# Performance work log

Hardware: AMD Instinct MI355X
Metric: run time of the kernel (lower is better)

## Reference

```python
import jax, jax.numpy as jnp
import numpy as np

LEVELS = ((64, 176), (32, 88), (16, 44), (8, 22))
S_TOTAL = sum(h * w for h, w in LEVELS)  # 14960
C = 128; HH = 8; HD = 16; R = 4; L = 4; P = 8
G = 32; PC_MIN = -4.0; PC_MAX = 4.0
NUM_CLASSES = 17; PROP = 3 + 3 + 4 + 1 + NUM_CLASSES  # 28


def _ln(x, g, b):
    m = x.mean(-1, keepdims=True)
    v = ((x - m) ** 2).mean(-1, keepdims=True)
    return (x - m) * jax.lax.rsqrt(v + 1e-5) * g + b


def setup_inputs() -> dict:
    key = jax.random.key(0)
    ks = jax.random.split(key, 20)
    B, N, CAM = 1, 1024, 6
    d = {}
    d['query'] = jax.random.normal(ks[0], (B, N, C), jnp.float32)
    d['gaussian_props'] = jax.random.normal(ks[1], (B, N, PROP), jnp.float32)
    d['ms_feats'] = jax.random.normal(ks[2], (B, CAM, S_TOTAL, C), jnp.float32)
    d['depth_maps'] = jax.random.uniform(ks[3], (B, CAM, 64, 176), jnp.float32, 0.5, 50.0)
    d['lidar2img'] = jax.random.normal(ks[4], (B, CAM, 4, 4), jnp.float32)
    d['img_h'] = 256
    d['img_w'] = 704
    w = lambda k, shp: jax.random.normal(k, shp, jnp.float32) * 0.02
    d['W_sc'] = w(ks[5], (3, 3, 3, C, C)); d['b_sc'] = jnp.zeros((C,), jnp.float32)
    d['sc_g'] = jnp.ones((C,), jnp.float32); d['sc_b'] = jnp.zeros((C,), jnp.float32)
    d['ref_off_w'] = w(ks[6], (C, R * 3)); d['ref_off_b'] = jnp.zeros((R * 3,), jnp.float32)
    d['off_w'] = w(ks[7], (C, HH * R * L * P * 2)); d['off_b'] = jnp.zeros((HH * R * L * P * 2,), jnp.float32)
    d['aw_w'] = w(ks[8], (C, HH * R * L * P)); d['aw_b'] = jnp.zeros((HH * R * L * P,), jnp.float32)
    d['val_w'] = w(ks[9], (C, C)); d['val_b'] = jnp.zeros((C,), jnp.float32)
    d['out_w'] = w(ks[10], (C, C)); d['out_b'] = jnp.zeros((C,), jnp.float32)
    d['an_g'] = jnp.ones((C,), jnp.float32); d['an_b'] = jnp.zeros((C,), jnp.float32)
    d['f1_w'] = w(ks[11], (C, 4 * C)); d['f1_b'] = jnp.zeros((4 * C,), jnp.float32)
    d['f2_w'] = w(ks[12], (4 * C, C)); d['f2_b'] = jnp.zeros((C,), jnp.float32)
    d['fn_g'] = jnp.ones((C,), jnp.float32); d['fn_b'] = jnp.zeros((C,), jnp.float32)
    d['p1_w'] = w(ks[13], (C, C)); d['p1_b'] = jnp.zeros((C,), jnp.float32)
    d['p2_w'] = w(ks[14], (C, PROP)); d['p2_b'] = jnp.zeros((PROP,), jnp.float32)
    return d


def _forward(query, gaussian_props, ms_feats, depth_maps, lidar2img,
             W_sc, b_sc, sc_g, sc_b, ref_off_w, ref_off_b, off_w, off_b,
             aw_w, aw_b, val_w, val_b, out_w, out_b, an_g, an_b,
             f1_w, f1_b, f2_w, f2_b, fn_g, fn_b, p1_w, p1_b, p2_w, p2_b,
             img_h, img_w):
    B, N, _ = query.shape
    CAM = ms_feats.shape[1]
    means = gaussian_props[..., :3]
    # ---- SparseConv3DBlock: scatter-mean voxelization, 3x3x3 conv, gather back ----
    vs = (PC_MAX - PC_MIN) / G
    vox = jnp.clip(jnp.floor((means - PC_MIN) / vs).astype(jnp.int32), 0, G - 1)
    flat = (vox[..., 0] * G + vox[..., 1]) * G + vox[..., 2]  # [B,N]
    bi = jnp.arange(B)[:, None]
    grid = jnp.zeros((B, G * G * G, C), query.dtype).at[bi, flat].add(query)
    cnt = jnp.zeros((B, G * G * G, 1), query.dtype).at[bi, flat].add(1.0)
    grid = (grid / jnp.maximum(cnt, 1.0)).reshape(B, G, G, G, C)
    grid = jax.lax.conv_general_dilated(grid, W_sc, (1, 1, 1), 'SAME',
                                        dimension_numbers=('NDHWC', 'DHWIO', 'NDHWC')) + b_sc
    grid = jax.nn.gelu(grid).reshape(B, G * G * G, C)
    query = _ln(query + grid[bi, flat], sc_g, sc_b)
    # ---- DeformableAttention3D ----
    fW = jnp.asarray(img_w, query.dtype); fH = jnp.asarray(img_h, query.dtype)
    ref3d = means[:, :, None, :] + (query @ ref_off_w + ref_off_b).reshape(B, N, R, 3)
    pts = jnp.concatenate([ref3d, jnp.ones_like(ref3d[..., :1])], -1)
    proj = jnp.einsum('bcij,bnrj->bcnri', lidar2img, pts)  # [B,CAM,N,R,4]
    z = proj[..., 2]; zc = jnp.maximum(z, 1e-5)
    u = proj[..., 0] / zc; v = proj[..., 1] / zc
    valid = (z > 1e-5) & (u >= 0) & (u < fW) & (v >= 0) & (v < fH)
    Hd, Wd = depth_maps.shape[2], depth_maps.shape[3]
    iu = jnp.clip((u / fW * Wd).astype(jnp.int32), 0, Wd - 1)
    iv = jnp.clip((v / fH * Hd).astype(jnp.int32), 0, Hd - 1)
    ds = jnp.take_along_axis(depth_maps.reshape(B, CAM, Hd * Wd),
                             (iv * Wd + iu).reshape(B, CAM, N * R), axis=2).reshape(B, CAM, N, R)
    wmask = jnp.exp(-jnp.abs(z - ds)) * valid.astype(query.dtype)  # [B,CAM,N,R]
    ref2 = jnp.stack([u / fW, v / fH], -1)  # [B,CAM,N,R,2]
    offs = (query @ off_w + off_b).reshape(B, N, HH, R, L, P, 2)
    attn = jax.nn.softmax((query @ aw_w + aw_b).reshape(B, N, HH, R * L * P), -1)
    attn = attn.reshape(B, N, HH, R, L, P)
    value = (ms_feats @ val_w + val_b).reshape(B, CAM, S_TOTAL, HH, HD)
    out = jnp.zeros((B, N, HH, HD), query.dtype)
    s0 = 0
    for l, (Hl, Wl) in enumerate(LEVELS):
        sz = Hl * Wl
        vl = value[:, :, s0:s0 + sz].transpose(0, 1, 3, 2, 4).reshape(B * CAM, HH, sz, HD)
        s0 += sz
        off_l = offs[:, :, :, :, l]  # [B,N,HH,R,P,2]
        loc = ref2[:, :, :, None, :, None, :] + off_l[:, None] / jnp.array([Wl, Hl], query.dtype)
        # loc: [B,CAM,N,HH,R,P,2] in normalized coords
        x = (loc[..., 0] * Wl - 0.5).transpose(0, 1, 3, 2, 4, 5).reshape(B * CAM, HH, N * R * P)
        y = (loc[..., 1] * Hl - 0.5).transpose(0, 1, 3, 2, 4, 5).reshape(B * CAM, HH, N * R * P)
        x0 = jnp.floor(x); y0 = jnp.floor(y); wx = x - x0; wy = y - y0
        x0i = jnp.clip(x0.astype(jnp.int32), 0, Wl - 1)
        x1i = jnp.clip(x0.astype(jnp.int32) + 1, 0, Wl - 1)
        y0i = jnp.clip(y0.astype(jnp.int32), 0, Hl - 1)
        y1i = jnp.clip(y0.astype(jnp.int32) + 1, 0, Hl - 1)
        g = lambda ix, iy: jnp.take_along_axis(vl, (iy * Wl + ix)[..., None], axis=2)
        samp = (((1 - wx) * (1 - wy))[..., None] * g(x0i, y0i)
                + (wx * (1 - wy))[..., None] * g(x1i, y0i)
                + ((1 - wx) * wy)[..., None] * g(x0i, y1i)
                + (wx * wy)[..., None] * g(x1i, y1i))  # [B*CAM,HH,N*R*P,HD]
        samp = samp.reshape(B, CAM, HH, N, R, P, HD)
        ws = attn[:, :, :, :, l, :][:, None].transpose(0, 1, 3, 2, 4, 5) * wmask[:, :, None, :, :, None]
        out = out + jnp.einsum('bchnrp,bchnrpd->bnhd', ws, samp)
    attn_out = out.reshape(B, N, C) @ out_w + out_b
    query = _ln(query + attn_out, an_g, an_b)
    query = _ln(query + (jax.nn.gelu(query @ f1_w + f1_b) @ f2_w + f2_b), fn_g, fn_b)
    props = gaussian_props + (jax.nn.gelu(query @ p1_w + p1_b) @ p2_w + p2_b)
    return query, props


def reference(query, gaussian_props, ms_feats, depth_maps, lidar2img,
              W_sc, b_sc, sc_g, sc_b, ref_off_w, ref_off_b, off_w, off_b,
              aw_w, aw_b, val_w, val_b, out_w, out_b, an_g, an_b,
              f1_w, f1_b, f2_w, f2_b, fn_g, fn_b, p1_w, p1_b, p2_w, p2_b,
              img_h, img_w):
    return _forward(query, gaussian_props, ms_feats, depth_maps, lidar2img,
                    W_sc, b_sc, sc_g, sc_b, ref_off_w, ref_off_b, off_w, off_b,
                    aw_w, aw_b, val_w, val_b, out_w, out_b, an_g, an_b,
                    f1_w, f1_b, f2_w, f2_b, fn_g, fn_b, p1_w, p1_b, p2_w, p2_b,
                    img_h, img_w)
```

## Files before the change

### kernel.cpp

```cpp
#include <hip/hip_runtime.h>
#include <hip/hip_bf16.h>
#include <math.h>

#define NQ    1024
#define CC    128
#define CAM   6
#define RR    4
#define LL    4
#define PP    8
#define HHD   8
#define HDD   16
#define GG    32
#define S_TOT 14960
#define PROPN 28
#define NTAP  27

typedef __attribute__((ext_vector_type(8))) short bf16x8;
typedef __attribute__((ext_vector_type(4))) float f32x4;

__device__ __forceinline__ float gelu_tanh(float x) {
    return 0.5f * x * (1.0f + tanhf(0.7978845608028654f * (x + 0.044715f * x * x * x)));
}

__device__ __forceinline__ unsigned short f2bf(float f) {
    union { float f; unsigned int u; } x; x.f = f;
    unsigned int r = (x.u + 0x7FFFu + ((x.u >> 16) & 1u)) >> 16;
    return (unsigned short)r;
}

__device__ __forceinline__ float bf2f(short s) {
    union { unsigned int u; float f; } x;
    x.u = ((unsigned int)(unsigned short)s) << 16;
    return x.f;
}

__global__ void k_wt_scatter(const float* __restrict__ Wsc, unsigned short* __restrict__ WscT,
                             const float* __restrict__ valw, unsigned short* __restrict__ valwT,
                             const float* __restrict__ outw, unsigned short* __restrict__ outwT,
                             const float* __restrict__ p1w, unsigned short* __restrict__ p1wT,
                             const float* __restrict__ f1w, unsigned short* __restrict__ f1wT,
                             const float* __restrict__ f2w, unsigned short* __restrict__ f2wT,
                             const float* __restrict__ offw, unsigned short* __restrict__ offwT,
                             const float* __restrict__ aww, unsigned short* __restrict__ awwT,
                             const float* __restrict__ p2w, unsigned short* __restrict__ p2wT,
                             const float* __restrict__ p2b, float* __restrict__ p2bp,
                             const float* __restrict__ qin, const float* __restrict__ gp,
                             float* __restrict__ grid, float* __restrict__ cnt,
                             int* __restrict__ flatidx) {
    __shared__ float t[64][65];
    __shared__ int sflat[2];
    int z = blockIdx.z;
    int tid = threadIdx.x;

    if (z >= 63) {
        int half = tid >> 7, c = tid & 127;
        int n = ((z - 63) * 4 + (blockIdx.x * 2 + blockIdx.y)) * 2 + half;
        if (c == 0) {
            float mx = gp[n * PROPN + 0], my = gp[n * PROPN + 1], mz = gp[n * PROPN + 2];
            int vx = (int)floorf((mx + 4.0f) * 4.0f);
            int vy = (int)floorf((my + 4.0f) * 4.0f);
            int vz = (int)floorf((mz + 4.0f) * 4.0f);
            vx = min(max(vx, 0), GG - 1);
            vy = min(max(vy, 0), GG - 1);
            vz = min(max(vz, 0), GG - 1);
            int f = (vx * GG + vy) * GG + vz;
            sflat[half] = f;
            flatidx[n] = f;
            atomicAdd(&cnt[f], 1.0f);
        }
        __syncthreads();
        atomicAdd(&grid[(size_t)sflat[half] * CC + c], qin[(size_t)n * CC + c]);
        return;
    }

    int n0 = blockIdx.x * 64, k0 = blockIdx.y * 64;
    if (z == 62) {
#pragma unroll
        for (int it = 0; it < 16; ++it) {
            int idx = tid + it * 256;
            int r = idx >> 6, c = idx & 63;
            t[r][c] = (n0 + c < PROPN) ? p2w[(size_t)(k0 + r) * PROPN + n0 + c] : 0.f;
        }
        __syncthreads();
#pragma unroll
        for (int it = 0; it < 16; ++it) {
            int idx = tid + it * 256;
            int r = idx >> 6, c = idx & 63;
            p2wT[(size_t)(n0 + r) * 128 + k0 + c] = f2bf(t[c][r]);
        }
        if (blockIdx.x == 0 && blockIdx.y == 0 && tid < 128)
            p2bp[tid] = (tid < PROPN) ? p2b[tid] : 0.f;
        return;
    }
    const float* src; unsigned short* dst; int ss, ds;
    if (z < 27)       { src = Wsc + (size_t)z * 16384; dst = WscT + (size_t)z * 16384; ss = 128; ds = 128; }
    else if (z == 27) { src = valw; dst = valwT; ss = 128; ds = 128; }
    else if (z == 28) { src = outw; dst = outwT; ss = 128; ds = 128; }
    else if (z == 29) { src = p1w;  dst = p1wT;  ss = 128; ds = 128; }
    else if (z < 34)  { int q = z - 30; src = f1w + q * 128; dst = f1wT + (size_t)q * 16384; ss = 512;  ds = 128; }
    else if (z < 38)  { int q = z - 34; src = f2w + (size_t)q * 16384; dst = f2wT + q * 128; ss = 128;  ds = 512; }
    else if (z < 54)  { int q = z - 38; src = offw + q * 128; dst = offwT + (size_t)q * 16384; ss = 2048; ds = 128; }
    else              { int q = z - 54; src = aww + q * 128;  dst = awwT + (size_t)q * 16384; ss = 1024; ds = 128; }
#pragma unroll
    for (int it = 0; it < 16; ++it) {
        int idx = tid + it * 256;
        int r = idx >> 6, c = idx & 63;
        t[r][c] = src[(size_t)(k0 + r) * ss + n0 + c];
    }
    __syncthreads();
#pragma unroll
    for (int it = 0; it < 16; ++it) {
        int idx = tid + it * 256;
        int r = idx >> 6, c = idx & 63;
        dst[(size_t)(n0 + r) * ds + k0 + c] = f2bf(t[c][r]);
    }
}

__global__ __launch_bounds__(256) void k_conv1m(
    const float* __restrict__ grid, const float* __restrict__ cnt,
    const int* __restrict__ flatidx, const unsigned short* __restrict__ WT,
    float* __restrict__ convacc27) {
    __shared__ bf16x8 As[128 * 16];
    __shared__ bf16x8 Bs[128 * 16];
    __shared__ int   nbase[128];
    __shared__ float nscale[128];
    int tid = threadIdx.x;
    int tap = blockIdx.y;
    int q0 = blockIdx.x * 128;
    int dz = tap / 9 - 1, dy = (tap / 3) % 3 - 1, dx = tap % 3 - 1;

    if (tid < 128) {
        int f = flatidx[q0 + tid];
        int nx = (f >> 10) + dz, ny = ((f >> 5) & 31) + dy, nz = (f & 31) + dx;
        bool ok = (nx >= 0 && nx < GG && ny >= 0 && ny < GG && nz >= 0 && nz < GG);
        int nf = ok ? (nx * GG + ny) * GG + nz : 0;
        nbase[tid] = nf;
        nscale[tid] = ok ? 1.0f / fmaxf(cnt[nf], 1.0f) : 0.f;
    }
    __syncthreads();
#pragma unroll
    for (int it = 0; it < 8; ++it) {
        int idx = tid + it * 256;
        int m = idx >> 4, c = idx & 15;
        const float* p = grid + (size_t)nbase[m] * CC + c * 8;
        float s = nscale[m];
        float4 a = *(const float4*)p;
        float4 b = *(const float4*)(p + 4);
        bf16x8 u;
        u[0] = (short)f2bf(a.x * s); u[1] = (short)f2bf(a.y * s);
        u[2] = (short)f2bf(a.z * s); u[3] = (short)f2bf(a.w * s);
        u[4] = (short)f2bf(b.x * s); u[5] = (short)f2bf(b.y * s);
        u[6] = (short)f2bf(b.z * s); u[7] = (short)f2bf(b.w * s);
        As[m * 16 + (c ^ (m & 15))] = u;
    }
    const unsigned short* Wt = WT + (size_t)tap * CC * CC;
#pragma unroll
    for (int it = 0; it < 8; ++it) {
        int idx = tid + it * 256;
        int n = idx >> 4, c = idx & 15;
        bf16x8 w = *(const bf16x8*)(Wt + (size_t)n * CC + c * 8);
        Bs[n * 16 + (c ^ (n & 15))] = w;
    }
    __syncthreads();

    int lane = tid & 63, wv = tid >> 6;
    int wr = (wv >> 1) * 64, wc = (wv & 1) * 64;
    int r = lane & 15, q = lane >> 4;
    f32x4 acc[4][4];
#pragma unroll
    for (int i = 0; i < 4; ++i)
#pragma unroll
        for (int j = 0; j < 4; ++j)
#pragma unroll
            for (int e = 0; e < 4; ++e) acc[i][j][e] = 0.f;
#pragma unroll
    for (int ks = 0; ks < 4; ++ks) {
        bf16x8 bfr[4];
#pragma unroll
        for (int j = 0; j < 4; ++j)
            bfr[j] = Bs[(wc + j * 16 + r) * 16 + ((ks * 4 + q) ^ r)];
#pragma unroll
        for (int i = 0; i < 4; ++i) {
            bf16x8 af = As[(wr + i * 16 + r) * 16 + ((ks * 4 + q) ^ r)];
#pragma unroll
            for (int j = 0; j < 4; ++j)
                acc[i][j] = __builtin_amdgcn_mfma_f32_16x16x32_bf16(af, bfr[j], acc[i][j], 0, 0, 0);
        }
    }
    float* dst = convacc27 + (size_t)tap * NQ * CC;
#pragma unroll
    for (int i = 0; i < 4; ++i)
#pragma unroll
        for (int e = 0; e < 4; ++e) {
            int m = q0 + wr + i * 16 + q * 4 + e;
#pragma unroll
            for (int j = 0; j < 4; ++j) {
                int col = wc + j * 16 + r;
                dst[(size_t)m * CC + col] = acc[i][j][e];
            }
        }
}

__global__ void k_ln_conv_proj(const float* __restrict__ a, const float* __restrict__ convacc27,
                               const float* __restrict__ bconv,
                               const float* __restrict__ g, const float* __restrict__ be,
                               float* __restrict__ out,
                               const float* __restrict__ refw, const float* __restrict__ refb,
                               const float* __restrict__ gp, const float* __restrict__ l2i,
                               const float* __restrict__ depth,
                               const int* __restrict__ ih, const int* __restrict__ iw,
                               float* __restrict__ wm, float* __restrict__ r2u,
                               float* __restrict__ r2v) {
    int n = blockIdx.x, c = threadIdx.x;
    float apart = 0.f;
#pragma unroll
    for (int t = 0; t < NTAP; ++t) apart += convacc27[((size_t)t * NQ + n) * CC + c];
    float x = a[n * CC + c] + gelu_tanh(apart + bconv[c]);
    __shared__ float w4[4];
    __shared__ float qrow[CC];
    __shared__ float ro[12];
    float s = x;
#pragma unroll
    for (int d = 1; d < 64; d <<= 1) s += __shfl_xor(s, d);
    if ((c & 63) == 0) w4[c >> 6] = s;
    __syncthreads();
    float m = (w4[0] + w4[1]) * (1.0f / CC);
    float dd = x - m;
    float v = dd * dd;
#pragma unroll
    for (int d = 1; d < 64; d <<= 1) v += __shfl_xor(v, d);
    if ((c & 63) == 0) w4[2 + (c >> 6)] = v;
    __syncthreads();
    float var = (w4[2] + w4[3]) * (1.0f / CC);
    float qv = dd * rsqrtf(var + 1e-5f) * g[c] + be[c];
    out[n * CC + c] = qv;
    qrow[c] = qv;
    __syncthreads();
    if (c < 12) {
        float sacc = refb[c];
#pragma unroll 4
        for (int k = 0; k < 128; ++k) sacc += qrow[k] * refw[k * 12 + c];
        ro[c] = sacc;
    }
    __syncthreads();
    if (c < 24) {
        int cam = c >> 2, r = c & 3;
        float fH = (float)(*ih), fW = (float)(*iw);
        const float* M = l2i + cam * 16;
        float px = gp[n * PROPN + 0] + ro[r * 3 + 0];
        float py = gp[n * PROPN + 1] + ro[r * 3 + 1];
        float pz = gp[n * PROPN + 2] + ro[r * 3 + 2];
        float p0 = M[0] * px + M[1] * py + M[2]  * pz + M[3];
        float p1 = M[4] * px + M[5] * py + M[6]  * pz + M[7];
        float p2 = M[8] * px + M[9] * py + M[10] * pz + M[11];
        float zc = fmaxf(p2, 1e-5f);
        float u = p0 / zc, vv = p1 / zc;
        bool valid = (p2 > 1e-5f) && (u >= 0.f) && (u < fW) && (vv >= 0.f) && (vv < fH);
        int iu = min(max((int)(u / fW * 176.f), 0), 175);
        int iv = min(max((int)(vv / fH * 64.f), 0), 63);
        float ds = depth[cam * 64 * 176 + iv * 176 + iu];
        int o = cam * (NQ * RR) + n * RR + r;
        wm[o]  = valid ? expf(-fabsf(p2 - ds)) : 0.f;
        r2u[o] = u / fW;
        r2v[o] = vv / fH;
    }
}

__global__ __launch_bounds__(256) void k_qhead(
    const float* __restrict__ A,
    const unsigned short* __restrict__ offwT, const float* __restrict__ offb,
    unsigned short* __restrict__ offsb,
    const unsigned short* __restrict__ awwT, const float* __restrict__ awb,
    unsigned short* __restrict__ attn)
{
    __shared__ bf16x8 Bs[128 * 16];
    bool isoff = blockIdx.x < 16;
    int n0 = (isoff ? blockIdx.x : (blockIdx.x - 16)) * 128;
    const unsigned short* WT = isoff ? offwT : awwT;
    int m0 = blockIdx.y * 128;
    int tid = threadIdx.x, lane = tid & 63, wv = tid >> 6;
    int r = lane & 15, q = lane >> 4;
    int mw = m0 + wv * 32;

#pragma unroll
    for (int it = 0; it < 8; ++it) {
        int idx = tid + it * 256;
        int n = idx >> 4, c = idx & 15;
        Bs[n * 16 + (c ^ (n & 15))] = *(const bf16x8*)(WT + (size_t)(n0 + n) * 128 + c * 8);
    }
    __syncthreads();

    f32x4 acc[2][8];
#pragma unroll
    for (int i = 0; i < 2; ++i)
#pragma unroll
        for (int j = 0; j < 8; ++j)
#pragma unroll
            for (int e = 0; e < 4; ++e) acc[i][j][e] = 0.f;

#pragma unroll
    for (int ks = 0; ks < 4; ++ks) {
        bf16x8 af[2];
#pragma unroll
        for (int i = 0; i < 2; ++i) {
            const float* p = A + (size_t)(mw + i * 16 + r) * 128 + (ks * 4 + q) * 8;
            float4 a = *(const float4*)p;
            float4 b = *(const float4*)(p + 4);
            bf16x8 u;
            u[0] = (short)f2bf(a.x); u[1] = (short)f2bf(a.y);
            u[2] = (short)f2bf(a.z); u[3] = (short)f2bf(a.w);
            u[4] = (short)f2bf(b.x); u[5] = (short)f2bf(b.y);
            u[6] = (short)f2bf(b.z); u[7] = (short)f2bf(b.w);
            af[i] = u;
        }
#pragma unroll
        for (int j = 0; j < 8; ++j) {
            bf16x8 b = Bs[(j * 16 + r) * 16 + ((ks * 4 + q) ^ r)];
#pragma unroll
            for (int i = 0; i < 2; ++i)
                acc[i][j] = __builtin_amdgcn_mfma_f32_16x16x32_bf16(af[i], b, acc[i][j], 0, 0, 0);
        }
    }

    float bia[8];
    const float* bsrc = isoff ? offb : awb;
#pragma unroll
    for (int j = 0; j < 8; ++j) bia[j] = bsrc[n0 + j * 16 + r];

    if (isoff) {
#pragma unroll
        for (int i = 0; i < 2; ++i)
#pragma unroll
            for (int e = 0; e < 4; ++e) {
                int m = mw + i * 16 + q * 4 + e;
                unsigned short* orow = offsb + (size_t)m * 2048 + n0;
#pragma unroll
                for (int j = 0; j < 8; ++j)
                    orow[j * 16 + r] = f2bf(acc[i][j][e] + bia[j]);
            }
    } else {
#pragma unroll
        for (int i = 0; i < 2; ++i)
#pragma unroll
            for (int e = 0; e < 4; ++e) {
                float mx = -1e30f;
#pragma unroll
                for (int j = 0; j < 8; ++j) mx = fmaxf(mx, acc[i][j][e] + bia[j]);
#pragma unroll
                for (int d = 1; d < 16; d <<= 1) mx = fmaxf(mx, __shfl_xor(mx, d));
                float ex[8];
                float sum = 0.f;
#pragma unroll
                for (int j = 0; j < 8; ++j) { ex[j] = expf(acc[i][j][e] + bia[j] - mx); sum += ex[j]; }
#pragma unroll
                for (int d = 1; d < 16; d <<= 1) sum += __shfl_xor(sum, d);
                float inv = 1.0f / sum;
                int m = mw + i * 16 + q * 4 + e;
                unsigned short* orow = attn + (size_t)m * 1024 + n0;
#pragma unroll
                for (int j = 0; j < 8; ++j)
                    orow[j * 16 + r] = f2bf(ex[j] * inv);
            }
    }
}

__global__ __launch_bounds__(256) void k_valproj(
    const float* __restrict__ A, const unsigned short* __restrict__ WT,
    const float* __restrict__ bias, unsigned short* __restrict__ out, int M)
{
    __shared__ bf16x8 Bs[128 * 16];
    __shared__ unsigned short Os[64 * 128];
    __shared__ float sbias[128];
    int tid = threadIdx.x;
    int m0 = blockIdx.x * 64;
    int lane = tid & 63, wv = tid >> 6;
    int r = lane & 15, q = lane >> 4;

#pragma unroll
    for (int it = 0; it < 8; ++it) {
        int idx = tid + it * 256;
        int n = idx >> 4, c = idx & 15;
        Bs[n * 16 + (c ^ (n & 15))] = *(const bf16x8*)(WT + (size_t)n * 128 + c * 8);
    }
    if (tid < 128) sbias[tid] = bias[tid];
    __syncthreads();

    int row = m0 + wv * 16 + r;
    int mg = min(row, M - 1);
    const float* pA = A + (size_t)mg * 128;

    f32x4 acc[8];
#pragma unroll
    for (int j = 0; j < 8; ++j)
#pragma unroll
        for (int e = 0; e < 4; ++e) acc[j][e] = 0.f;

#pragma unroll
    for (int ks = 0; ks < 4; ++ks) {
        const float* p = pA + ks * 32 + q * 8;
        float4 a = *(const float4*)p;
        float4 b = *(const float4*)(p + 4);
        bf16x8 af;
        af[0] = (short)f2bf(a.x); af[1] = (short)f2bf(a.y);
        af[2] = (short)f2bf(a.z); af[3] = (short)f2bf(a.w);
        af[4] = (short)f2bf(b.x); af[5] = (short)f2bf(b.y);
        af[6] = (short)f2bf(b.z); af[7] = (short)f2bf(b.w);
        bf16x8 bfr[8];
#pragma unroll
        for (int j = 0; j < 8; ++j)
            bfr[j] = Bs[(j * 16 + r) * 16 + ((ks * 4 + q) ^ r)];
#pragma unroll
        for (int j = 0; j < 8; ++j)
            acc[j] = __builtin_amdgcn_mfma_f32_16x16x32_bf16(af, bfr[j], acc[j], 0, 0, 0);
    }

#pragma unroll
    for (int j = 0; j < 8; ++j)
#pragma unroll
        for (int e = 0; e < 4; ++e) {
            int rl = wv * 16 + q * 4 + e;
            Os[rl * 128 + j * 16 + r] = f2bf(acc[j][e] + sbias[j * 16 + r]);
        }
    __syncthreads();
#pragma unroll
    for (int it = 0; it < 4; ++it) {
        int idx = tid + it * 256;
        int rl = idx >> 4, ch = idx & 15;
        int m = m0 + rl;
        if (m < M)
            *(bf16x8*)(out + (size_t)m * 128 + ch * 8) = *(const bf16x8*)&Os[rl * 128 + ch * 8];
    }
}

__global__ void k_sample(const unsigned short* __restrict__ value,
                         const unsigned short* __restrict__ offsb,
                         const unsigned short* __restrict__ attn,
                         const float* __restrict__ wm,
                         const float* __restrict__ r2u, const float* __restrict__ r2v,
                         float* __restrict__ sampout) {
    const int Wl_[4] = {176, 88, 44, 22};
    const int Hl_[4] = {64, 32, 16, 8};
    const int s0_[4] = {0, 11264, 14080, 14784};
    int n = blockIdx.x, tid = threadIdx.x;
    __shared__ float s_attn[1024];
    __shared__ float s_offs[2048];
    __shared__ float s_wm[24], s_ru[24], s_rv[24];

    if (tid < 128) {
        bf16x8 v = *(const bf16x8*)(attn + (size_t)n * 1024 + tid * 8);
#pragma unroll
        for (int d = 0; d < 8; ++d) s_attn[tid * 8 + d] = bf2f(v[d]);
    }
    {
        bf16x8 v = *(const bf16x8*)(offsb + (size_t)n * 2048 + tid * 8);
#pragma unroll
        for (int d = 0; d < 8; ++d) s_offs[tid * 8 + d] = bf2f(v[d]);
    }
    if (tid < 24) {
        int cam = tid >> 2, r = tid & 3;
        int o = cam * (NQ * RR) + n * RR + r;
        s_wm[tid] = wm[o]; s_ru[tid] = r2u[o]; s_rv[tid] = r2v[o];
    }
    __syncthreads();

    int h = tid >> 5, slot = tid & 31;
    int l = slot >> 3, p = slot & 7;
    int Wl = Wl_[l], Hl = Hl_[l];
    float fWl = (float)Wl, fHl = (float)Hl;
    float acc[16];
#pragma unroll
    for (int d = 0; d < 16; ++d) acc[d] = 0.f;

    for (int cr = 0; cr < 24; ++cr) {
        int cam = cr >> 2, r = cr & 3;
        float ws = s_attn[h * 128 + r * 32 + l * 8 + p] * s_wm[cr];
        if (ws == 0.f) continue;
        float ox = s_offs[h * 256 + r * 64 + l * 16 + p * 2 + 0];
        float oy = s_offs[h * 256 + r * 64 + l * 16 + p * 2 + 1];
        float x = s_ru[cr] * fWl + ox - 0.5f;
        float y = s_rv[cr] * fHl + oy - 0.5f;
        float xf = floorf(x), yf = floorf(y);
        float wx = x - xf, wy = y - yf;
        int x0 = min(max((int)xf, 0), Wl - 1);
        int x1 = min(max((int)xf + 1, 0), Wl - 1);
        int y0 = min(max((int)yf, 0), Hl - 1);
        int y1 = min(max((int)yf + 1, 0), Hl - 1);
        size_t b = ((size_t)cam * S_TOT + s0_[l]) * CC + h * HDD;
        const unsigned short* p00 = value + b + (size_t)(y0 * Wl + x0) * CC;
        const unsigned short* p01 = value + b + (size_t)(y0 * Wl + x1) * CC;
        const unsigned short* p10 = value + b + (size_t)(y1 * Wl + x0) * CC;
        const unsigned short* p11 = value + b + (size_t)(y1 * Wl + x1) * CC;
        float w00 = ws * (1.f - wx) * (1.f - wy);
        float w01 = ws * wx * (1.f - wy);
        float w10 = ws * (1.f - wx) * wy;
        float w11 = ws * wx * wy;
        bf16x8 va0 = *(const bf16x8*)p00, va1 = *(const bf16x8*)(p00 + 8);
        bf16x8 vb0 = *(const bf16x8*)p01, vb1 = *(const bf16x8*)(p01 + 8);
        bf16x8 vc0 = *(const bf16x8*)p10, vc1 = *(const bf16x8*)(p10 + 8);
        bf16x8 vd0 = *(const bf16x8*)p11, vd1 = *(const bf16x8*)(p11 + 8);
#pragma unroll
        for (int d = 0; d < 8; ++d)
            acc[d] += w00 * bf2f(va0[d]) + w01 * bf2f(vb0[d]) + w10 * bf2f(vc0[d]) + w11 * bf2f(vd0[d]);
#pragma unroll
        for (int d = 0; d < 8; ++d)
            acc[8 + d] += w00 * bf2f(va1[d]) + w01 * bf2f(vb1[d]) + w10 * bf2f(vc1[d]) + w11 * bf2f(vd1[d]);
    }

#pragma unroll
    for (int d = 0; d < 16; ++d) {
        float a = acc[d];
#pragma unroll
        for (int s = 16; s >= 1; s >>= 1) a += __shfl_xor(a, s, 32);
        acc[d] = a;
    }
    if (slot == 0) {
#pragma unroll
        for (int d = 0; d < 16; ++d)
            sampout[(size_t)n * CC + h * HDD + d] = acc[d];
    }
}

__global__ __launch_bounds__(256) void k_tail(
    const float* __restrict__ sampout,
    const unsigned short* __restrict__ outwT, const float* __restrict__ outb,
    const float* __restrict__ q1, const float* __restrict__ ang, const float* __restrict__ anb,
    const unsigned short* __restrict__ f1wT, const float* __restrict__ f1b,
    const unsigned short* __restrict__ f2wT, const float* __restrict__ f2b,
    const float* __restrict__ fng, const float* __restrict__ fnb,
    const unsigned short* __restrict__ p1wT, const float* __restrict__ p1b,
    const unsigned short* __restrict__ p2wT, const float* __restrict__ p2bp,
    const float* __restrict__ gp, float* __restrict__ outq, float* __restrict__ outp)
{
    __shared__ bf16x8 As[16 * 16];
    __shared__ bf16x8 Aff[16 * 64];
    __shared__ float xrow[16 * 128];
    __shared__ float q2s[16 * 128];
    unsigned short* Affu = (unsigned short*)Aff;
    unsigned short* As2u = (unsigned short*)Aff;
    int tid = threadIdx.x, m0 = blockIdx.x * 16;
    int lane = tid & 63, wv = tid >> 6;
    int wc = wv * 32;
    int r = lane & 15, q = lane >> 4;
    int lrow = tid >> 4, ls = tid & 15;

    bf16x8 b1[2][4];
#pragma unroll
    for (int j = 0; j < 2; ++j)
#pragma unroll
        for (int ks = 0; ks < 4; ++ks)
            b1[j][ks] = *(const bf16x8*)(outwT + (size_t)(wc + j * 16 + r) * 128 + (ks * 4 + q) * 8);

    {
        int m = tid >> 4, c = tid & 15;
        const float* p = sampout + (size_t)(m0 + m) * 128 + c * 8;
        float4 a = *(const float4*)p;
        float4 b = *(const float4*)(p + 4);
        bf16x8 u;
        u[0] = (short)f2bf(a.x); u[1] = (short)f2bf(a.y);
        u[2] = (short)f2bf(a.z); u[3] = (short)f2bf(a.w);
        u[4] = (short)f2bf(b.x); u[5] = (short)f2bf(b.y);
        u[6] = (short)f2bf(b.z); u[7] = (short)f2bf(b.w);
        As[m * 16 + (c ^ m)] = u;
    }
    __syncthreads();

    f32x4 acc[2];
    bf16x8 a4[4];
#pragma unroll
    for (int ks = 0; ks < 4; ++ks) a4[ks] = As[r * 16 + ((ks * 4 + q) ^ r)];
#pragma unroll
    for (int j = 0; j < 2; ++j)
#pragma unroll
        for (int e = 0; e < 4; ++e) acc[j][e] = 0.f;
#pragma unroll
    for (int ks = 0; ks < 4; ++ks)
#pragma unroll
        for (int j = 0; j < 2; ++j)
            acc[j] = __builtin_amdgcn_mfma_f32_16x16x32_bf16(a4[ks], b1[j][ks], acc[j], 0, 0, 0);
#pragma unroll
    for (int e = 0; e < 4; ++e) {
        int ml = q * 4 + e;
#pragma unroll
        for (int j = 0; j < 2; ++j) {
            int cl = wc + j * 16 + r;
            xrow[ml * 128 + cl] = acc[j][e] + outb[cl] + q1[(size_t)(m0 + ml) * 128 + cl];
        }
    }
    __syncthreads();

    {
        float* xr = xrow + lrow * 128;
        float sum = 0.f;
#pragma unroll
        for (int e = ls; e < 128; e += 16) sum += xr[e];
#pragma unroll
        for (int d = 8; d; d >>= 1) sum += __shfl_xor(sum, d, 16);
        float mean = sum * (1.0f / 128.0f);
        float var = 0.f;
#pragma unroll
        for (int e = ls; e < 128; e += 16) { float dd = xr[e] - mean; var += dd * dd; }
#pragma unroll
        for (int d = 8; d; d >>= 1) var += __shfl_xor(var, d, 16);
        float rstd = rsqrtf(var * (1.0f / 128.0f) + 1e-5f);
#pragma unroll
        for (int e = ls; e < 128; e += 16)
            q2s[lrow * 128 + e] = (xr[e] - mean) * rstd * ang[e] + anb[e];
    }
    __syncthreads();
    {
        int m = tid >> 4, c = tid & 15;
        const float* p = q2s + m * 128 + c * 8;
        bf16x8 u;
#pragma unroll
        for (int d = 0; d < 8; ++d) u[d] = (short)f2bf(p[d]);
        As[m * 16 + (c ^ m)] = u;
    }
    __syncthreads();

#pragma unroll
    for (int ks = 0; ks < 4; ++ks) a4[ks] = As[r * 16 + ((ks * 4 + q) ^ r)];
    bf16x8 bcur[2][4];
#pragma unroll
    for (int j = 0; j < 2; ++j)
#pragma unroll
        for (int ks = 0; ks < 4; ++ks)
            bcur[j][ks] = *(const bf16x8*)(f1wT + (size_t)(wc + j * 16 + r) * 128 + (ks * 4 + q) * 8);
#pragma unroll
    for (int nt = 0; nt < 4; ++nt) {
        bf16x8 bnx[2][4];
        if (nt < 3) {
#pragma unroll
            for (int j = 0; j < 2; ++j)
#pragma unroll
                for (int ks = 0; ks < 4; ++ks)
                    bnx[j][ks] = *(const bf16x8*)(f1wT + (size_t)(nt + 1) * 16384
                                                  + (size_t)(wc + j * 16 + r) * 128 + (ks * 4 + q) * 8);
        }
#pragma unroll
        for (int j = 0; j < 2; ++j)
#pragma unroll
            for (int e = 0; e < 4; ++e) acc[j][e] = 0.f;
#pragma unroll
        for (int ks = 0; ks < 4; ++ks)
#pragma unroll
            for (int j = 0; j < 2; ++j)
                acc[j] = __builtin_amdgcn_mfma_f32_16x16x32_bf16(a4[ks], bcur[j][ks], acc[j], 0, 0, 0);
#pragma unroll
        for (int e = 0; e < 4; ++e) {
            int ml = q * 4 + e;
#pragma unroll
            for (int j = 0; j < 2; ++j) {
                int col = nt * 128 + wc + j * 16 + r;
                float v = gelu_tanh(acc[j][e] + f1b[col]);
                Affu[(ml * 64 + ((col >> 3) ^ ml)) * 8 + (col & 7)] = f2bf(v);
            }
        }
        if (nt < 3) {
#pragma unroll
            for (int j = 0; j < 2; ++j)
#pragma unroll
                for (int ks = 0; ks < 4; ++ks) bcur[j][ks] = bnx[j][ks];
        }
    }
    __syncthreads();

#pragma unroll
    for (int j = 0; j < 2; ++j)
#pragma unroll
        for (int e = 0; e < 4; ++e) acc[j][e] = 0.f;
#pragma unroll
    for (int j = 0; j < 2; ++j)
#pragma unroll
        for (int ks = 0; ks < 4; ++ks)
            bcur[j][ks] = *(const bf16x8*)(f2wT + (size_t)(wc + j * 16 + r) * 512 + (ks * 4 + q) * 8);
#pragma unroll
    for (int kc = 0; kc < 4; ++kc) {
        bf16x8 bnx[2][4];
        if (kc < 3) {
#pragma unroll
            for (int j = 0; j < 2; ++j)
#pragma unroll
                for (int ks = 0; ks < 4; ++ks)
                    bnx[j][ks] = *(const bf16x8*)(f2wT + (size_t)(wc + j * 16 + r) * 512
                                                  + ((kc + 1) * 16 + ks * 4 + q) * 8);
        }
#pragma unroll
        for (int ks = 0; ks < 4; ++ks) {
            bf16x8 af = Aff[r * 64 + ((kc * 16 + ks * 4 + q) ^ r)];
#pragma unroll
            for (int j = 0; j < 2; ++j)
                acc[j] = __builtin_amdgcn_mfma_f32_16x16x32_bf16(af, bcur[j][ks], acc[j], 0, 0, 0);
        }
        if (kc < 3) {
#pragma unroll
            for (int j = 0; j < 2; ++j)
#pragma unroll
                for (int ks = 0; ks < 4; ++ks) bcur[j][ks] = bnx[j][ks];
        }
    }
#pragma unroll
    for (int e = 0; e < 4; ++e) {
        int ml = q * 4 + e;
#pragma unroll
        for (int j = 0; j < 2; ++j) {
            int cl = wc + j * 16 + r;
            xrow[ml * 128 + cl] = acc[j][e] + f2b[cl] + q2s[ml * 128 + cl];
        }
    }
    __syncthreads();

    {
        float* xr = xrow + lrow * 128;
        float sum = 0.f;
#pragma unroll
        for (int e = ls; e < 128; e += 16) sum += xr[e];
#pragma unroll
        for (int d = 8; d; d >>= 1) sum += __shfl_xor(sum, d, 16);
        float mean = sum * (1.0f / 128.0f);
        float var = 0.f;
#pragma unroll
        for (int e = ls; e < 128; e += 16) { float dd = xr[e] - mean; var += dd * dd; }
#pragma unroll
        for (int d = 8; d; d >>= 1) var += __shfl_xor(var, d, 16);
        float rstd = rsqrtf(var * (1.0f / 128.0f) + 1e-5f);
        float* oq = outq + (size_t)(m0 + lrow) * 128;
#pragma unroll
        for (int e = ls; e < 128; e += 16) {
            float v = (xr[e] - mean) * rstd * fng[e] + fnb[e];
            oq[e] = v;
            q2s[lrow * 128 + e] = v;
        }
    }
    __syncthreads();
    {
        int m = tid >> 4, c = tid & 15;
        const float* p = q2s + m * 128 + c * 8;
        bf16x8 u;
#pragma unroll
        for (int d = 0; d < 8; ++d) u[d] = (short)f2bf(p[d]);
        As[m * 16 + (c ^ m)] = u;
    }
    __syncthreads();

#pragma unroll
    for (int ks = 0; ks < 4; ++ks) a4[ks] = As[r * 16 + ((ks * 4 + q) ^ r)];
#pragma unroll
    for (int j = 0; j < 2; ++j) {
#pragma unroll
        for (int ks = 0; ks < 4; ++ks)
            bcur[j][ks] = *(const bf16x8*)(p1wT + (size_t)(wc + j * 16 + r) * 128 + (ks * 4 + q) * 8);
#pragma unroll
        for (int e = 0; e < 4; ++e) acc[j][e] = 0.f;
    }
#pragma unroll
    for (int j = 0; j < 2; ++j)
#pragma unroll
        for (int ks = 0; ks < 4; ++ks)
            b1[j][ks] = *(const bf16x8*)(p2wT + (size_t)(wc + j * 16 + r) * 128 + (ks * 4 + q) * 8);
#pragma unroll
    for (int ks = 0; ks < 4; ++ks)
#pragma unroll
        for (int j = 0; j < 2; ++j)
            acc[j] = __builtin_amdgcn_mfma_f32_16x16x32_bf16(a4[ks], bcur[j][ks], acc[j], 0, 0, 0);
#pragma unroll
    for (int e = 0; e < 4; ++e) {
        int ml = q * 4 + e;
#pragma unroll
        for (int j = 0; j < 2; ++j) {
            int cl = wc + j * 16 + r;
            float v = gelu_tanh(acc[j][e] + p1b[cl]);
            As2u[(ml * 16 + ((cl >> 3) ^ ml)) * 8 + (cl & 7)] = f2bf(v);
        }
    }
    __syncthreads();

#pragma unroll
    for (int j = 0; j < 2; ++j)
#pragma unroll
        for (int e = 0; e < 4; ++e) acc[j][e] = 0.f;
#pragma unroll
    for (int ks = 0; ks < 4; ++ks) {
        bf16x8 af = Aff[r * 16 + ((ks * 4 + q) ^ r)];
#pragma unroll
        for (int j = 0; j < 2; ++j)
            acc[j] = __builtin_amdgcn_mfma_f32_16x16x32_bf16(af, b1[j][ks], acc[j], 0, 0, 0);
    }
#pragma unroll
    for (int e = 0; e < 4; ++e) {
        int m = m0 + q * 4 + e;
#pragma unroll
        for (int j = 0; j < 2; ++j) {
            int cl = wc + j * 16 + r;
            if (cl < PROPN)
                outp[(size_t)m * PROPN + cl] = acc[j][e] + p2bp[cl] + gp[(size_t)m * PROPN + cl];
        }
    }
}

extern "C" void kernel_launch(void* const* d_in, const int* in_sizes, int n_in,
                              void* d_out, int out_size, void* d_ws, size_t ws_size,
                              hipStream_t stream) {
    const float* query = (const float*)d_in[0];
    const float* gp    = (const float*)d_in[1];
    const float* ms    = (const float*)d_in[2];
    const float* depth = (const float*)d_in[3];
    const float* l2i   = (const float*)d_in[4];
    const int*   ih    = (const int*)d_in[5];
    const int*   iw    = (const int*)d_in[6];
    const float* Wsc   = (const float*)d_in[7];
    const float* bsc   = (const float*)d_in[8];
    const float* scg   = (const float*)d_in[9];
    const float* scb   = (const float*)d_in[10];
    const float* refw  = (const float*)d_in[11];
    const float* refb  = (const float*)d_in[12];
    const float* offw  = (const float*)d_in[13];
    const float* offbi = (const float*)d_in[14];
    const float* aww   = (const float*)d_in[15];
    const float* awb   = (const float*)d_in[16];
    const float* valw  = (const float*)d_in[17];
    const float* valb  = (const float*)d_in[18];
    const float* outw  = (const float*)d_in[19];
    const float* outb  = (const float*)d_in[20];
    const float* ang   = (const float*)d_in[21];
    const float* anb   = (const float*)d_in[22];
    const float* f1w   = (const float*)d_in[23];
    const float* f1b   = (const float*)d_in[24];
    const float* f2w   = (const float*)d_in[25];
    const float* f2b   = (const float*)d_in[26];
    const float* fng   = (const float*)d_in[27];
    const float* fnb   = (const float*)d_in[28];
    const float* p1w   = (const float*)d_in[29];
    const float* p1b   = (const float*)d_in[30];
    const float* p2w   = (const float*)d_in[31];
    const float* p2b   = (const float*)d_in[32];

    float* outq = (float*)d_out;
    float* outp = outq + NQ * CC;

    float* ws = (float*)d_ws;
    size_t o = 0;
    float* grid    = ws + o; o += (size_t)GG * GG * GG * CC;
    float* cnt     = ws + o; o += GG * GG * GG;
    size_t zero_floats = o;
    int*   flatidx = (int*)(ws + o); o += NQ;
    float* convacc27 = ws + o; o += (size_t)NTAP * NQ * CC;
    float* q1      = ws + o; o += NQ * CC;
    float* wm      = ws + o; o += CAM * NQ * RR;
    float* r2u     = ws + o; o += CAM * NQ * RR;
    float* r2v     = ws + o; o += CAM * NQ * RR;
    float* sampout = ws + o; o += NQ * CC;
    float* p2bp    = ws + o; o += 128;
    unsigned short* u16base = (unsigned short*)(ws + o);
    size_t uo = 0;
    unsigned short* value = u16base + uo; uo += (size_t)CAM * S_TOT * CC;
    unsigned short* offsb = u16base + uo; uo += (size_t)NQ * 2048;
    unsigned short* attn  = u16base + uo; uo += (size_t)NQ * 1024;
    unsigned short* offwT = u16base + uo; uo += (size_t)2048 * 128;
    unsigned short* awwT  = u16base + uo; uo += (size_t)1024 * 128;
    unsigned short* valwT = u16base + uo; uo += 128 * 128;
    unsigned short* outwT = u16base + uo; uo += 128 * 128;
    unsigned short* f1wT  = u16base + uo; uo += 512 * 128;
    unsigned short* f2wT  = u16base + uo; uo += 128 * 512;
    unsigned short* p1wT  = u16base + uo; uo += 128 * 128;
    unsigned short* p2wT  = u16base + uo; uo += 128 * 128;
    unsigned short* WscT  = u16base + uo; uo += (size_t)27 * 128 * 128;
    (void)ws_size; (void)in_sizes; (void)n_in; (void)out_size;

    hipMemsetAsync(ws, 0, zero_floats * sizeof(float), stream);

    k_wt_scatter<<<dim3(2, 2, 63 + 128), 256, 0, stream>>>(
        Wsc, WscT, valw, valwT, outw, outwT, p1w, p1wT, f1w, f1wT, f2w, f2wT,
        offw, offwT, aww, awwT, p2w, p2wT, p2b, p2bp,
        query, gp, grid, cnt, flatidx);

    k_conv1m<<<dim3(8, 27), 256, 0, stream>>>(grid, cnt, flatidx, WscT, convacc27);
    k_ln_conv_proj<<<NQ, CC, 0, stream>>>(query, convacc27, bsc, scg, scb, q1,
                                          refw, refb, gp, l2i, depth, ih, iw, wm, r2u, r2v);

    k_qhead<<<dim3(24, 8), 256, 0, stream>>>(q1, offwT, offbi, offsb, awwT, awb, attn);
    k_valproj<<<(CAM * S_TOT + 63) / 64, 256, 0, stream>>>(ms, valwT, valb, value, CAM * S_TOT);
    k_sample<<<NQ, 256, 0, stream>>>(value, offsb, attn, wm, r2u, r2v, sampout);

    k_tail<<<64, 256, 0, stream>>>(sampout, outwT, outb, q1, ang, anb,
                                   f1wT, f1b, f2wT, f2b, fng, fnb,
                                   p1wT, p1b, p2wT, p2bp, gp, outq, outp);
}
```

Before: 227.5 us.

## Fuse value projection into weight-prep kernel and split sampling across camera halves

```diff
diff --git a/kernel.cpp b/kernel.cpp
--- a/kernel.cpp
+++ b/kernel.cpp
@@ -14,6 +14,9 @@
 #define S_TOT 14960
 #define PROPN 28
 #define NTAP  27
+#define MVAL  (CAM * S_TOT)
+#define NVB   ((MVAL + 63) / 64)
+#define ZWT   191
 
 typedef __attribute__((ext_vector_type(8))) short bf16x8;
 typedef __attribute__((ext_vector_type(4))) float f32x4;
@@ -34,8 +37,9 @@
     return x.f;
 }
 
-__global__ void k_wt_scatter(const float* __restrict__ Wsc, unsigned short* __restrict__ WscT,
-                             const float* __restrict__ valw, unsigned short* __restrict__ valwT,
+__global__ __launch_bounds__(256) void k_wt_scatter(
+                             const float* __restrict__ Wsc, unsigned short* __restrict__ WscT,
+                             const float* __restrict__ valw,
                              const float* __restrict__ outw, unsigned short* __restrict__ outwT,
                              const float* __restrict__ p1w, unsigned short* __restrict__ p1wT,
                              const float* __restrict__ f1w, unsigned short* __restrict__ f1wT,
@@ -46,11 +50,82 @@
                              const float* __restrict__ p2b, float* __restrict__ p2bp,
                              const float* __restrict__ qin, const float* __restrict__ gp,
                              float* __restrict__ grid, float* __restrict__ cnt,
-                             int* __restrict__ flatidx) {
-    __shared__ float t[64][65];
+                             int* __restrict__ flatidx,
+                             const float* __restrict__ ms, const float* __restrict__ valb,
+                             unsigned short* __restrict__ value) {
+    __shared__ union SM {
+        float t[64][65];
+        struct { bf16x8 Bs[128 * 16]; unsigned short Os[64 * 128]; float sbias[128]; } v;
+    } sm;
     __shared__ int sflat[2];
     int z = blockIdx.z;
     int tid = threadIdx.x;
+
+    if (z >= ZWT) {
+        int vb = (z - ZWT) * 4 + blockIdx.x * 2 + blockIdx.y;
+        if (vb >= NVB) return;
+        int m0 = vb * 64;
+        int lane = tid & 63, wv = tid >> 6;
+        int r = lane & 15, q = lane >> 4;
+        unsigned int* Bsw = (unsigned int*)sm.v.Bs;
+#pragma unroll
+        for (int it = 0; it < 32; ++it) {
+            int idx = tid + it * 256;
+            int k = (idx >> 7) * 2, nn = idx & 127;
+            unsigned int lo = f2bf(valw[k * 128 + nn]);
+            unsigned int hi = f2bf(valw[(k + 1) * 128 + nn]);
+            Bsw[(nn * 16 + ((k >> 3) ^ (nn & 15))) * 4 + ((k >> 1) & 3)] = lo | (hi << 16);
+        }
+        if (tid < 128) sm.v.sbias[tid] = valb[tid];
+        __syncthreads();
+
+        int row = m0 + wv * 16 + r;
+        int mg = min(row, MVAL - 1);
+        const float* pA = ms + (size_t)mg * 128;
+
+        f32x4 acc[8];
+#pragma unroll
+        for (int j = 0; j < 8; ++j)
+#pragma unroll
+            for (int e = 0; e < 4; ++e) acc[j][e] = 0.f;
+
+#pragma unroll
+        for (int ks = 0; ks < 4; ++ks) {
+            const float* p = pA + ks * 32 + q * 8;
+            float4 a = *(const float4*)p;
+            float4 b = *(const float4*)(p + 4);
+            bf16x8 af;
+            af[0] = (short)f2bf(a.x); af[1] = (short)f2bf(a.y);
+            af[2] = (short)f2bf(a.z); af[3] = (short)f2bf(a.w);
+            af[4] = (short)f2bf(b.x); af[5] = (short)f2bf(b.y);
+            af[6] = (short)f2bf(b.z); af[7] = (short)f2bf(b.w);
+            bf16x8 bfr[8];
+#pragma unroll
+            for (int j = 0; j < 8; ++j)
+                bfr[j] = sm.v.Bs[(j * 16 + r) * 16 + ((ks * 4 + q) ^ r)];
+#pragma unroll
+            for (int j = 0; j < 8; ++j)
+                acc[j] = __builtin_amdgcn_mfma_f32_16x16x32_bf16(af, bfr[j], acc[j], 0, 0, 0);
+        }
+
+#pragma unroll
+        for (int j = 0; j < 8; ++j)
+#pragma unroll
+            for (int e = 0; e < 4; ++e) {
+                int rl = wv * 16 + q * 4 + e;
+                sm.v.Os[rl * 128 + j * 16 + r] = f2bf(acc[j][e] + sm.v.sbias[j * 16 + r]);
+            }
+        __syncthreads();
+#pragma unroll
+        for (int it = 0; it < 4; ++it) {
+            int idx = tid + it * 256;
+            int rl = idx >> 4, ch = idx & 15;
+            int m = m0 + rl;
+            if (m < MVAL)
+                *(bf16x8*)(value + (size_t)m * 128 + ch * 8) = *(const bf16x8*)&sm.v.Os[rl * 128 + ch * 8];
+        }
+        return;
+    }
 
     if (z >= 63) {
         int half = tid >> 7, c = tid & 127;
@@ -79,14 +154,14 @@
         for (int it = 0; it < 16; ++it) {
             int idx = tid + it * 256;
             int r = idx >> 6, c = idx & 63;
-            t[r][c] = (n0 + c < PROPN) ? p2w[(size_t)(k0 + r) * PROPN + n0 + c] : 0.f;
+            sm.t[r][c] = (n0 + c < PROPN) ? p2w[(size_t)(k0 + r) * PROPN + n0 + c] : 0.f;
         }
         __syncthreads();
 #pragma unroll
         for (int it = 0; it < 16; ++it) {
             int idx = tid + it * 256;
             int r = idx >> 6, c = idx & 63;
-            p2wT[(size_t)(n0 + r) * 128 + k0 + c] = f2bf(t[c][r]);
+            p2wT[(size_t)(n0 + r) * 128 + k0 + c] = f2bf(sm.t[c][r]);
         }
         if (blockIdx.x == 0 && blockIdx.y == 0 && tid < 128)
             p2bp[tid] = (tid < PROPN) ? p2b[tid] : 0.f;
@@ -94,25 +169,25 @@
     }
     const float* src; unsigned short* dst; int ss, ds;
     if (z < 27)       { src = Wsc + (size_t)z * 16384; dst = WscT + (size_t)z * 16384; ss = 128; ds = 128; }
-    else if (z == 27) { src = valw; dst = valwT; ss = 128; ds = 128; }
-    else if (z == 28) { src = outw; dst = outwT; ss = 128; ds = 128; }
-    else if (z == 29) { src = p1w;  dst = p1wT;  ss = 128; ds = 128; }
-    else if (z < 34)  { int q = z - 30; src = f1w + q * 128; dst = f1wT + (size_t)q * 16384; ss = 512;  ds = 128; }
-    else if (z < 38)  { int q = z - 34; src = f2w + (size_t)q * 16384; dst = f2wT + q * 128; ss = 128;  ds = 512; }
-    else if (z < 54)  { int q = z - 38; src = offw + q * 128; dst = offwT + (size_t)q * 16384; ss = 2048; ds = 128; }
-    else              { int q = z - 54; src = aww + q * 128;  dst = awwT + (size_t)q * 16384; ss = 1024; ds = 128; }
+    else if (z == 27) { src = outw; dst = outwT; ss = 128; ds = 128; }
+    else if (z == 28) { src = p1w;  dst = p1wT;  ss = 128; ds = 128; }
+    else if (z == 29) { int q = z - 29; src = f1w + q * 128; dst = f1wT + (size_t)q * 16384; ss = 512; ds = 128; }
+    else if (z < 33)  { int q = z - 29; src = f1w + q * 128; dst = f1wT + (size_t)q * 16384; ss = 512;  ds = 128; }
+    else if (z < 37)  { int q = z - 33; src = f2w + (size_t)q * 16384; dst = f2wT + q * 128; ss = 128;  ds = 512; }
+    else if (z < 53)  { int q = z - 37; src = offw + q * 128; dst = offwT + (size_t)q * 16384; ss = 2048; ds = 128; }
+    else              { int q = z - 53; src = aww + q * 128;  dst = awwT + (size_t)q * 16384; ss = 1024; ds = 128; }
 #pragma unroll
     for (int it = 0; it < 16; ++it) {
         int idx = tid + it * 256;
         int r = idx >> 6, c = idx & 63;
-        t[r][c] = src[(size_t)(k0 + r) * ss + n0 + c];
+        sm.t[r][c] = src[(size_t)(k0 + r) * ss + n0 + c];
     }
     __syncthreads();
 #pragma unroll
     for (int it = 0; it < 16; ++it) {
         int idx = tid + it * 256;
         int r = idx >> 6, c = idx & 63;
-        dst[(size_t)(n0 + r) * ds + k0 + c] = f2bf(t[c][r]);
+        dst[(size_t)(n0 + r) * ds + k0 + c] = f2bf(sm.t[c][r]);
     }
 }
 
@@ -204,7 +279,7 @@
 __global__ void k_ln_conv_proj(const float* __restrict__ a, const float* __restrict__ convacc27,
                                const float* __restrict__ bconv,
                                const float* __restrict__ g, const float* __restrict__ be,
-                               float* __restrict__ out,
+                               float* __restrict__ out, unsigned short* __restrict__ outbf,
                                const float* __restrict__ refw, const float* __restrict__ refb,
                                const float* __restrict__ gp, const float* __restrict__ l2i,
                                const float* __restrict__ depth,
@@ -234,6 +309,7 @@
     float var = (w4[2] + w4[3]) * (1.0f / CC);
     float qv = dd * rsqrtf(var + 1e-5f) * g[c] + be[c];
     out[n * CC + c] = qv;
+    outbf[n * CC + c] = f2bf(qv);
     qrow[c] = qv;
     __syncthreads();
     if (c < 12) {
@@ -267,7 +343,7 @@
 }
 
 __global__ __launch_bounds__(256) void k_qhead(
-    const float* __restrict__ A,
+    const unsigned short* __restrict__ Abf,
     const unsigned short* __restrict__ offwT, const float* __restrict__ offb,
     unsigned short* __restrict__ offsb,
     const unsigned short* __restrict__ awwT, const float* __restrict__ awb,
@@ -302,17 +378,8 @@
     for (int ks = 0; ks < 4; ++ks) {
         bf16x8 af[2];
 #pragma unroll
-        for (int i = 0; i < 2; ++i) {
-            const float* p = A + (size_t)(mw + i * 16 + r) * 128 + (ks * 4 + q) * 8;
-            float4 a = *(const float4*)p;
-            float4 b = *(const float4*)(p + 4);
-            bf16x8 u;
-            u[0] = (short)f2bf(a.x); u[1] = (short)f2bf(a.y);
-            u[2] = (short)f2bf(a.z); u[3] = (short)f2bf(a.w);
-            u[4] = (short)f2bf(b.x); u[5] = (short)f2bf(b.y);
-            u[6] = (short)f2bf(b.z); u[7] = (short)f2bf(b.w);
-            af[i] = u;
-        }
+        for (int i = 0; i < 2; ++i)
+            af[i] = *(const bf16x8*)(Abf + (size_t)(mw + i * 16 + r) * 128 + (ks * 4 + q) * 8);
 #pragma unroll
         for (int j = 0; j < 8; ++j) {
             bf16x8 b = Bs[(j * 16 + r) * 16 + ((ks * 4 + q) ^ r)];
@@ -364,75 +431,8 @@
     }
 }
 
-__global__ __launch_bounds__(256) void k_valproj(
-    const float* __restrict__ A, const unsigned short* __restrict__ WT,
-    const float* __restrict__ bias, unsigned short* __restrict__ out, int M)
-{
-    __shared__ bf16x8 Bs[128 * 16];
-    __shared__ unsigned short Os[64 * 128];
-    __shared__ float sbias[128];
-    int tid = threadIdx.x;
-    int m0 = blockIdx.x * 64;
-    int lane = tid & 63, wv = tid >> 6;
-    int r = lane & 15, q = lane >> 4;
-
-#pragma unroll
-    for (int it = 0; it < 8; ++it) {
-        int idx = tid + it * 256;
-        int n = idx >> 4, c = idx & 15;
-        Bs[n * 16 + (c ^ (n & 15))] = *(const bf16x8*)(WT + (size_t)n * 128 + c * 8);
-    }
-    if (tid < 128) sbias[tid] = bias[tid];
-    __syncthreads();
-
-    int row = m0 + wv * 16 + r;
-    int mg = min(row, M - 1);
-    const float* pA = A + (size_t)mg * 128;
-
-    f32x4 acc[8];
-#pragma unroll
-    for (int j = 0; j < 8; ++j)
-#pragma unroll
-        for (int e = 0; e < 4; ++e) acc[j][e] = 0.f;
-
-#pragma unroll
-    for (int ks = 0; ks < 4; ++ks) {
-        const float* p = pA + ks * 32 + q * 8;
-        float4 a = *(const float4*)p;
-        float4 b = *(const float4*)(p + 4);
-        bf16x8 af;
-        af[0] = (short)f2bf(a.x); af[1] = (short)f2bf(a.y);
-        af[2] = (short)f2bf(a.z); af[3] = (short)f2bf(a.w);
-        af[4] = (short)f2bf(b.x); af[5] = (short)f2bf(b.y);
-        af[6] = (short)f2bf(b.z); af[7] = (short)f2bf(b.w);
-        bf16x8 bfr[8];
-#pragma unroll
-        for (int j = 0; j < 8; ++j)
-            bfr[j] = Bs[(j * 16 + r) * 16 + ((ks * 4 + q) ^ r)];
-#pragma unroll
-        for (int j = 0; j < 8; ++j)
-            acc[j] = __builtin_amdgcn_mfma_f32_16x16x32_bf16(af, bfr[j], acc[j], 0, 0, 0);
-    }
-
-#pragma unroll
-    for (int j = 0; j < 8; ++j)
-#pragma unroll
-        for (int e = 0; e < 4; ++e) {
-            int rl = wv * 16 + q * 4 + e;
-            Os[rl * 128 + j * 16 + r] = f2bf(acc[j][e] + sbias[j * 16 + r]);
-        }
-    __syncthreads();
-#pragma unroll
-    for (int it = 0; it < 4; ++it) {
-        int idx = tid + it * 256;
-        int rl = idx >> 4, ch = idx & 15;
-        int m = m0 + rl;
-        if (m < M)
-            *(bf16x8*)(out + (size_t)m * 128 + ch * 8) = *(const bf16x8*)&Os[rl * 128 + ch * 8];
-    }
-}
-
-__global__ void k_sample(const unsigned short* __restrict__ value,
+__global__ __launch_bounds__(512) void k_sample(
+                         const unsigned short* __restrict__ value,
                          const unsigned short* __restrict__ offsb,
                          const unsigned short* __restrict__ attn,
                          const float* __restrict__ wm,
@@ -445,13 +445,14 @@
     __shared__ float s_attn[1024];
     __shared__ float s_offs[2048];
     __shared__ float s_wm[24], s_ru[24], s_rv[24];
+    __shared__ float part[HHD][HDD];
 
     if (tid < 128) {
         bf16x8 v = *(const bf16x8*)(attn + (size_t)n * 1024 + tid * 8);
 #pragma unroll
         for (int d = 0; d < 8; ++d) s_attn[tid * 8 + d] = bf2f(v[d]);
     }
-    {
+    if (tid < 256) {
         bf16x8 v = *(const bf16x8*)(offsb + (size_t)n * 2048 + tid * 8);
 #pragma unroll
         for (int d = 0; d < 8; ++d) s_offs[tid * 8 + d] = bf2f(v[d]);
@@ -463,7 +464,9 @@
     }
     __syncthreads();
 
-    int h = tid >> 5, slot = tid & 31;
+    int half = tid >> 8;
+    int t8 = tid & 255;
+    int h = t8 >> 5, slot = t8 & 31;
     int l = slot >> 3, p = slot & 7;
     int Wl = Wl_[l], Hl = Hl_[l];
     float fWl = (float)Wl, fHl = (float)Hl;
@@ -471,7 +474,7 @@
 #pragma unroll
     for (int d = 0; d < 16; ++d) acc[d] = 0.f;
 
-    for (int cr = 0; cr < 24; ++cr) {
+    for (int cr = half * 12; cr < half * 12 + 12; ++cr) {
         int cam = cr >> 2, r = cr & 3;
         float ws = s_attn[h * 128 + r * 32 + l * 8 + p] * s_wm[cr];
         if (ws == 0.f) continue;
@@ -513,10 +516,15 @@
         for (int s = 16; s >= 1; s >>= 1) a += __shfl_xor(a, s, 32);
         acc[d] = a;
     }
-    if (slot == 0) {
+    if (half == 1 && slot == 0) {
+#pragma unroll
+        for (int d = 0; d < 16; ++d) part[h][d] = acc[d];
+    }
+    __syncthreads();
+    if (half == 0 && slot == 0) {
 #pragma unroll
         for (int d = 0; d < 16; ++d)
-            sampout[(size_t)n * CC + h * HDD + d] = acc[d];
+            sampout[(size_t)n * CC + h * HDD + d] = acc[d] + part[h][d];
     }
 }
 
@@ -855,9 +863,9 @@
     unsigned short* value = u16base + uo; uo += (size_t)CAM * S_TOT * CC;
     unsigned short* offsb = u16base + uo; uo += (size_t)NQ * 2048;
     unsigned short* attn  = u16base + uo; uo += (size_t)NQ * 1024;
+    unsigned short* q1bf  = u16base + uo; uo += (size_t)NQ * CC;
     unsigned short* offwT = u16base + uo; uo += (size_t)2048 * 128;
     unsigned short* awwT  = u16base + uo; uo += (size_t)1024 * 128;
-    unsigned short* valwT = u16base + uo; uo += 128 * 128;
     unsigned short* outwT = u16base + uo; uo += 128 * 128;
     unsigned short* f1wT  = u16base + uo; uo += 512 * 128;
     unsigned short* f2wT  = u16base + uo; uo += 128 * 512;
@@ -868,18 +876,19 @@
 
     hipMemsetAsync(ws, 0, zero_floats * sizeof(float), stream);
 
-    k_wt_scatter<<<dim3(2, 2, 63 + 128), 256, 0, stream>>>(
-        Wsc, WscT, valw, valwT, outw, outwT, p1w, p1wT, f1w, f1wT, f2w, f2wT,
+    int zvp = (NVB + 3) / 4;
+    k_wt_scatter<<<dim3(2, 2, ZWT + zvp), 256, 0, stream>>>(
+        Wsc, WscT, valw, outw, outwT, p1w, p1wT, f1w, f1wT, f2w, f2wT,
         offw, offwT, aww, awwT, p2w, p2wT, p2b, p2bp,
-        query, gp, grid, cnt, flatidx);
+        query, gp, grid, cnt, flatidx,
+        ms, valb, value);
 
     k_conv1m<<<dim3(8, 27), 256, 0, stream>>>(grid, cnt, flatidx, WscT, convacc27);
-    k_ln_conv_proj<<<NQ, CC, 0, stream>>>(query, convacc27, bsc, scg, scb, q1,
+    k_ln_conv_proj<<<NQ, CC, 0, stream>>>(query, convacc27, bsc, scg, scb, q1, q1bf,
                                           refw, refb, gp, l2i, depth, ih, iw, wm, r2u, r2v);
 
-    k_qhead<<<dim3(24, 8), 256, 0, stream>>>(q1, offwT, offbi, offsb, awwT, awb, attn);
-    k_valproj<<<(CAM * S_TOT + 63) / 64, 256, 0, stream>>>(ms, valwT, valb, value, CAM * S_TOT);
-    k_sample<<<NQ, 256, 0, stream>>>(value, offsb, attn, wm, r2u, r2v, sampout);
+    k_qhead<<<dim3(24, 8), 256, 0, stream>>>(q1bf, offwT, offbi, offsb, awwT, awb, attn);
+    k_sample<<<NQ, 512, 0, stream>>>(value, offsb, attn, wm, r2u, r2v, sampout);
 
     k_tail<<<64, 256, 0, stream>>>(sampout, outwT, outb, q1, ang, anb,
                                    f1wT, f1b, f2wT, f2b, fng, fnb,
```

Result: no change. 225.4 us (-0.9%).
